# Performance work log

Hardware: AMD Instinct MI355X
Metric: run time of the kernel (lower is better)

## Reference

```python
import jax, jax.numpy as jnp
import numpy as np

DIM, HEADS, WS, SS = 256, 8, 4, 2
B, D, H, W = 2, 16, 56, 56


def _rel_pos_index(ws):
    coords = np.stack(np.meshgrid(np.arange(ws), np.arange(ws), np.arange(ws), indexing='ij'))
    flat = coords.reshape(3, -1)                      # [3, n]
    rel = (flat[:, :, None] - flat[:, None, :]).transpose(1, 2, 0).astype(np.int64)  # [n,n,3]
    rel[..., 0] += ws - 1; rel[..., 1] += ws - 1; rel[..., 2] += ws - 1
    rel[..., 0] *= (2 * ws - 1) ** 2
    rel[..., 1] *= (2 * ws - 1)
    return rel.sum(-1)                                # [n, n]


def _attn_mask(d, h, w, ws, ss):
    # dims are divisible by ws here, so padded dims == dims (matches torch ceil-pad)
    img = np.zeros((d, h, w))
    sl = (slice(0, -ws), slice(-ws, -ss), slice(-ss, None))
    cnt = 0
    for dsl in sl:
        for hsl in sl:
            for wsl in sl:
                img[dsl, hsl, wsl] = cnt
                cnt += 1
    mw = img.reshape(d // ws, ws, h // ws, ws, w // ws, ws)
    mw = mw.transpose(0, 2, 4, 1, 3, 5).reshape(-1, ws ** 3)   # [nW, n]
    diff = mw[:, None, :] - mw[:, :, None]
    return np.where(diff != 0, -100.0, 0.0).astype(np.float32)  # [nW, n, n]


def _window_partition(x, ws):
    b, d, h, w, c = x.shape
    x = x.reshape(b, d // ws, ws, h // ws, ws, w // ws, ws, c)
    return x.transpose(0, 1, 3, 5, 2, 4, 6, 7).reshape(-1, ws ** 3, c)


def _window_reverse(win, ws, b, d, h, w, c):
    x = win.reshape(b, d // ws, h // ws, w // ws, ws, ws, ws, c)
    return x.transpose(0, 1, 4, 2, 5, 3, 6, 7).reshape(b, d, h, w, c)


def _ln(x, g, b, eps=1e-5):
    mu = x.mean(-1, keepdims=True)
    var = ((x - mu) ** 2).mean(-1, keepdims=True)
    return (x - mu) * jax.lax.rsqrt(var + eps) * g + b


def setup_inputs() -> dict:
    key = jax.random.key(0)
    ks = jax.random.split(key, 8)
    s = 0.02
    return {
        'x': jax.random.normal(ks[0], (B, D, H, W, DIM), jnp.float32),
        'norm1_g': jnp.ones((DIM,), jnp.float32),
        'norm1_b': jnp.zeros((DIM,), jnp.float32),
        'qkv_w': jax.random.normal(ks[1], (DIM, 3 * DIM), jnp.float32) * s,
        'qkv_b': jnp.zeros((3 * DIM,), jnp.float32),
        'proj_w': jax.random.normal(ks[2], (DIM, DIM), jnp.float32) * s,
        'proj_b': jnp.zeros((DIM,), jnp.float32),
        'rpb_table': jax.random.normal(ks[3], ((2 * WS - 1) ** 3, HEADS), jnp.float32) * s,
        'norm2_g': jnp.ones((DIM,), jnp.float32),
        'norm2_b': jnp.zeros((DIM,), jnp.float32),
        'fc1_w': jax.random.normal(ks[4], (DIM, 4 * DIM), jnp.float32) * s,
        'fc1_b': jnp.zeros((4 * DIM,), jnp.float32),
        'fc2_w': jax.random.normal(ks[5], (4 * DIM, DIM), jnp.float32) * s,
        'fc2_b': jnp.zeros((DIM,), jnp.float32),
    }


def reference(x, norm1_g, norm1_b, qkv_w, qkv_b, proj_w, proj_b, rpb_table,
              norm2_g, norm2_b, fc1_w, fc1_b, fc2_w, fc2_b):
    b, d, h, w, c = x.shape
    nh, ws, ss = HEADS, WS, SS
    hd = c // nh
    shortcut = x

    xn = _ln(x, norm1_g, norm1_b)
    xs = jnp.roll(xn, shift=(-ss, -ss, -ss), axis=(1, 2, 3))
    xw = _window_partition(xs, ws)            # [B_, n, c]
    B_, n, _ = xw.shape

    qkv = (xw @ qkv_w + qkv_b).reshape(B_, n, 3, nh, hd).transpose(2, 0, 3, 1, 4)
    q, k, v = qkv[0], qkv[1], qkv[2]          # [B_, nh, n, hd]
    attn = jnp.einsum('bhqd,bhkd->bhqk', q * (hd ** -0.5), k)

    rpi = jnp.asarray(_rel_pos_index(ws).reshape(-1))
    bias = rpb_table[rpi].reshape(n, n, nh).transpose(2, 0, 1)  # [nh, n, n]
    attn = attn + bias[None]

    mask = jnp.asarray(_attn_mask(d, h, w, ws, ss))             # [nW, n, n]
    nW = mask.shape[0]
    attn = attn.reshape(B_ // nW, nW, nh, n, n) + mask[None, :, None]
    attn = jax.nn.softmax(attn.reshape(B_, nh, n, n), axis=-1)

    out = jnp.einsum('bhqk,bhkd->bhqd', attn, v).transpose(0, 2, 1, 3).reshape(B_, n, c)
    out = out @ proj_w + proj_b

    xr = _window_reverse(out, ws, b, d, h, w, c)
    xr = jnp.roll(xr, shift=(ss, ss, ss), axis=(1, 2, 3))
    x1 = shortcut + xr

    y = _ln(x1, norm2_g, norm2_b)
    y = jax.nn.gelu(y @ fc1_w + fc1_b, approximate=False) @ fc2_w + fc2_b
    return x1 + y
```

## Files before the change

### kernel.cpp

```cpp
#include <hip/hip_runtime.h>
#include <math.h>


using f32x4  = __attribute__((ext_vector_type(4))) float;
using bf16x8 = __attribute__((ext_vector_type(8))) short;

#define MFMA16 __builtin_amdgcn_mfma_f32_16x16x32_bf16

__device__ __forceinline__ short f2bf(float f) {
  unsigned u = __builtin_bit_cast(unsigned, f);
  u += 0x7fffu + ((u >> 16) & 1u);
  return (short)(u >> 16);
}

__device__ __forceinline__ float gelu_f(float v) {
  const float u = 1.5957691216057308f * v * (1.f + 0.044715f * v * v);
  const float e = __expf(u);
  return v - v * __builtin_amdgcn_rcpf(e + 1.f);
}

#define GLDS16(g, l) __builtin_amdgcn_global_load_lds(                        \
    (__attribute__((address_space(1))) void*)(g),                             \
    (__attribute__((address_space(3))) void*)(l), 16, 0, 0)

__global__ void transpose_all_k(const float* __restrict__ qkv_w,
                                const float* __restrict__ proj_w,
                                const float* __restrict__ fc1_w,
                                const float* __restrict__ fc2_w,
                                short* __restrict__ o_qkv,
                                short* __restrict__ o_proj,
                                short* __restrict__ o_fc1,
                                short* __restrict__ o_fc2) {
  int bid = blockIdx.x;
  const float* in; short* out; int K, N;
  if (bid < 768)       { in = qkv_w;  out = o_qkv;  K = 256;  N = 768; }
  else if (bid < 1024) { in = proj_w; out = o_proj; K = 256;  N = 256;  bid -= 768; }
  else if (bid < 2048) { in = fc1_w;  out = o_fc1;  K = 256;  N = 1024; bid -= 1024; }
  else                 { in = fc2_w;  out = o_fc2;  K = 1024; N = 256;  bid -= 2048; }
  const int idx = bid * 256 + threadIdx.x;
  const int k = idx / N, n = idx % N;
  out[(size_t)n * K + k] = f2bf(in[idx]);
}

__global__ __launch_bounds__(256) void ln1_part_k(
    const float* __restrict__ x, const float* __restrict__ g,
    const float* __restrict__ bta, short* __restrict__ xw) {
  const int wave = threadIdx.x >> 6, lane = threadIdx.x & 63;
  const int row = blockIdx.x * 4 + wave;
  const int win = row >> 6, tok = row & 63;
  const int b = win / 784, wi = win % 784;
  const int wd = wi / 196, wh = (wi / 14) % 14, ww = wi % 14;
  const int tz = tok >> 4, ty = (tok >> 2) & 3, tx = tok & 3;
  const int gd = (wd * 4 + tz + 2) & 15;
  int gh = wh * 4 + ty + 2; if (gh >= 56) gh -= 56;
  int gw = ww * 4 + tx + 2; if (gw >= 56) gw -= 56;
  const size_t src = ((((size_t)b * 16 + gd) * 56 + gh) * 56 + gw) * 256;
  const float4 v = ((const float4*)(x + src))[lane];
  float s = v.x + v.y + v.z + v.w;
#pragma unroll
  for (int m = 1; m < 64; m <<= 1) s += __shfl_xor(s, m);
  const float mean = s * (1.f / 256.f);
  const float dx = v.x - mean, dy = v.y - mean, dz = v.z - mean, dw = v.w - mean;
  float q = dx * dx + dy * dy + dz * dz + dw * dw;
#pragma unroll
  for (int m = 1; m < 64; m <<= 1) q += __shfl_xor(q, m);
  const float rstd = rsqrtf(q * (1.f / 256.f) + 1e-5f);
  const float4 gg = ((const float4*)g)[lane];
  const float4 bb = ((const float4*)bta)[lane];
  short4 o;
  o.x = f2bf(dx * rstd * gg.x + bb.x);
  o.y = f2bf(dy * rstd * gg.y + bb.y);
  o.z = f2bf(dz * rstd * gg.z + bb.z);
  o.w = f2bf(dw * rstd * gg.w + bb.w);
  *(short4*)(xw + (size_t)row * 256 + lane * 4) = o;
}

__global__ __launch_bounds__(256) void ln2_k(
    const float* __restrict__ x1, const float* __restrict__ g,
    const float* __restrict__ bta, short* __restrict__ yn) {
  const int wave = threadIdx.x >> 6, lane = threadIdx.x & 63;
  const int row = blockIdx.x * 4 + wave;
  const float4 v = ((const float4*)(x1 + (size_t)row * 256))[lane];
  float s = v.x + v.y + v.z + v.w;
#pragma unroll
  for (int m = 1; m < 64; m <<= 1) s += __shfl_xor(s, m);
  const float mean = s * (1.f / 256.f);
  const float dx = v.x - mean, dy = v.y - mean, dz = v.z - mean, dw = v.w - mean;
  float q = dx * dx + dy * dy + dz * dz + dw * dw;
#pragma unroll
  for (int m = 1; m < 64; m <<= 1) q += __shfl_xor(q, m);
  const float rstd = rsqrtf(q * (1.f / 256.f) + 1e-5f);
  const float4 gg = ((const float4*)g)[lane];
  const float4 bb = ((const float4*)bta)[lane];
  short4 o;
  o.x = f2bf(dx * rstd * gg.x + bb.x);
  o.y = f2bf(dy * rstd * gg.y + bb.y);
  o.z = f2bf(dz * rstd * gg.z + bb.z);
  o.w = f2bf(dw * rstd * gg.w + bb.w);
  *(short4*)(yn + (size_t)row * 256 + lane * 4) = o;
}

template <int EPI, int XSWZ>
__global__ __launch_bounds__(256) void gemm_k(
    const short* __restrict__ A, const short* __restrict__ Bt,
    const float* __restrict__ bias, const float* __restrict__ resid,
    void* __restrict__ OutP, int N, int K) {
  __shared__ short SMEM[32768];
  const int tid = threadIdx.x;
  const int wave = tid >> 6, lane = tid & 63;
  const int quad = lane >> 4, l15 = lane & 15;
  int m0, n0;
  if constexpr (XSWZ) {
    const int gx = gridDim.x;
    int lin = blockIdx.y * gx + blockIdx.x;
    const int q8 = (gx * gridDim.y) >> 3;
    lin = (lin & 7) * q8 + (lin >> 3);
    m0 = (lin / gx) * 128;
    n0 = (lin % gx) * 128;
  } else {
    m0 = blockIdx.y * 128;
    n0 = blockIdx.x * 128;
  }
  const int wm = (wave >> 1) * 64, wn = (wave & 1) * 64;

  f32x4 acc[4][4] = {};

  auto stage = [&](int b, int kk) {
    short* Asb = SMEM + b * 16384;
    short* Bsb = Asb + 8192;
#pragma unroll
    for (int i = 0; i < 4; ++i) {
      const int p = wave * 256 + i * 64 + lane;
      const int row = p >> 3;
      const int c = (p & 7) ^ (row & 7);
      GLDS16(A  + (size_t)(m0 + row) * K + (kk + c * 8),
             Asb + (size_t)(wave * 256 + i * 64) * 8);
      GLDS16(Bt + (size_t)(n0 + row) * K + (kk + c * 8),
             Bsb + (size_t)(wave * 256 + i * 64) * 8);
    }
  };
  auto compute = [&](int b) {
    const short* Asb = SMEM + b * 16384;
    const short* Bsb = Asb + 8192;
#pragma unroll
    for (int ks = 0; ks < 2; ++ks) {
      bf16x8 af[4], bfr[4];
#pragma unroll
      for (int t = 0; t < 4; ++t) {
        const int ra = wm + t * 16 + l15;
        const int ca = (ks * 4 + quad) ^ (ra & 7);
        af[t] = *(const bf16x8*)(Asb + ra * 64 + ca * 8);
        const int rb = wn + t * 16 + l15;
        const int cb = (ks * 4 + quad) ^ (rb & 7);
        bfr[t] = *(const bf16x8*)(Bsb + rb * 64 + cb * 8);
      }
#pragma unroll
      for (int mt = 0; mt < 4; ++mt)
#pragma unroll
        for (int nt = 0; nt < 4; ++nt)
          acc[mt][nt] = MFMA16(af[mt], bfr[nt], acc[mt][nt], 0, 0, 0);
    }
  };

  stage(0, 0);
  __syncthreads();
  int cur = 0;
  const int NT = K >> 6;
  for (int t = 0; t < NT - 1; ++t) {
    stage(cur ^ 1, (t + 1) * 64);
    compute(cur);
    __syncthreads();
    cur ^= 1;
  }
  compute(cur);

  __syncthreads();
  if constexpr (EPI == 0 || EPI == 1) {
#pragma unroll
    for (int nt = 0; nt < 4; ++nt) {
      const int col = wn + nt * 16 + l15;
      const float bv = bias[n0 + col];
#pragma unroll
      for (int mt = 0; mt < 4; ++mt)
#pragma unroll
        for (int reg = 0; reg < 4; ++reg) {
          const int row = wm + mt * 16 + quad * 4 + reg;
          float v = acc[mt][nt][reg] + bv;
          if constexpr (EPI == 1) v = gelu_f(v);
          const int byte = (row << 8) | ((col << 1) ^ ((row & 7) << 4));
          *(short*)((char*)SMEM + byte) = f2bf(v);
        }
    }
    __syncthreads();
    short* out = (short*)OutP;
#pragma unroll
    for (int i = 0; i < 8; ++i) {
      const int off = i * 4096 + tid * 16;
      const int row = off >> 8;
      const bf16x8 val =
          *(const bf16x8*)((char*)SMEM + (off ^ ((row & 7) << 4)));
      if constexpr (EPI == 0) {
        const int colg = n0 + ((off & 255) >> 1);
        const int gq = colg >> 8, rem = colg & 255;
        const int hh = rem >> 5, dd = rem & 31;
        const int grow = m0 + row;
        const int win = grow >> 6, tok = grow & 63;
        *(bf16x8*)(out + ((((size_t)win * 8 + hh) * 3 + gq) << 11)
                       + tok * 32 + dd) = val;
      } else {
        *(bf16x8*)(out + (size_t)(m0 + row) * N + n0 + ((off & 255) >> 1)) = val;
      }
    }
  } else {
    float* out = (float*)OutP;
#pragma unroll
    for (int hh = 0; hh < 2; ++hh) {
      if (hh) __syncthreads();
      if (wm == hh * 64) {
#pragma unroll
        for (int nt = 0; nt < 4; ++nt) {
          const int col = wn + nt * 16 + l15;
          const float bv = bias[n0 + col];
#pragma unroll
          for (int mt = 0; mt < 4; ++mt)
#pragma unroll
            for (int reg = 0; reg < 4; ++reg) {
              const int rloc = mt * 16 + quad * 4 + reg;
              const int byte = (rloc << 9) | ((col << 2) ^ ((rloc & 7) << 4));
              *(float*)((char*)SMEM + byte) = acc[mt][nt][reg] + bv;
            }
        }
      }
      __syncthreads();
#pragma unroll
      for (int i = 0; i < 8; ++i) {
        const int off = i * 4096 + tid * 16;
        const int rloc = off >> 9;
        f32x4 val = *(const f32x4*)((char*)SMEM + (off ^ ((rloc & 7) << 4)));
        const int colf = (off & 511) >> 2;
        const int grow = m0 + hh * 64 + rloc;
        size_t dst;
        if constexpr (EPI == 2) {
          const int win = grow >> 6, tok = grow & 63;
          const int b = win / 784, wi = win % 784;
          const int wd = wi / 196, wh = (wi / 14) % 14, ww = wi % 14;
          const int tz = tok >> 4, ty = (tok >> 2) & 3, tx = tok & 3;
          const int gd = (wd * 4 + tz + 2) & 15;
          int gh = wh * 4 + ty + 2; if (gh >= 56) gh -= 56;
          int gw = ww * 4 + tx + 2; if (gw >= 56) gw -= 56;
          dst = ((((size_t)b * 16 + gd) * 56 + gh) * 56 + gw) * 256
                + n0 + colf;
        } else {
          dst = (size_t)grow * 256 + n0 + colf;
        }
        const f32x4 r = *(const f32x4*)(resid + dst);
        val = val + r;
        *(f32x4*)(out + dst) = val;
      }
    }
  }
}

__global__ __launch_bounds__(256) void attn_k(
    const short* __restrict__ qkv, const float* __restrict__ rpb,
    short* __restrict__ aout) {
  __shared__ short Plds[4 * 64 * 80];
  const int tid = threadIdx.x;
  const int wave = tid >> 6, lane = tid & 63;
  const int quad = lane >> 4, l15 = lane & 15;
  const int win = blockIdx.x >> 1;
  const int h = ((blockIdx.x & 1) << 2) + wave;
  const int wi = win % 784;
  const int wd = wi / 196, wh = (wi / 14) % 14, ww = wi % 14;
  const short* base = qkv + ((((size_t)win * 8 + h) * 3) << 11);

  bf16x8 qf[4], kf[4];
#pragma unroll
  for (int t = 0; t < 4; ++t) {
    qf[t] = *(const bf16x8*)(base + (t * 16 + l15) * 32 + quad * 8);
    kf[t] = *(const bf16x8*)(base + 2048 + (t * 16 + l15) * 32 + quad * 8);
  }
  f32x4 S[4][4] = {};
#pragma unroll
  for (int mt = 0; mt < 4; ++mt)
#pragma unroll
    for (int nt = 0; nt < 4; ++nt)
      S[mt][nt] = MFMA16(qf[mt], kf[nt], S[mt][nt], 0, 0, 0);

  const bool bd = (wd == 3), bh = (wh == 13), bw = (ww == 13);
  const int yc = l15 >> 2, xc = l15 & 3;
  int labc[4];
#pragma unroll
  for (int nt = 0; nt < 4; ++nt) {
    const int rd = bd ? (nt < 2 ? 1 : 2) : 0;
    const int rh = bh ? (yc < 2 ? 1 : 2) : 0;
    const int rw = bw ? (xc < 2 ? 1 : 2) : 0;
    labc[nt] = rd * 9 + rh * 3 + rw;
  }
  const float scale = 0.17677669529663687f;
#pragma unroll
  for (int mt = 0; mt < 4; ++mt) {
    const int rdr = bd ? (mt < 2 ? 1 : 2) : 0;
    const int rhr = bh ? (quad < 2 ? 1 : 2) : 0;
#pragma unroll
    for (int reg = 0; reg < 4; ++reg) {
      const int rwr = bw ? (reg < 2 ? 1 : 2) : 0;
      const int labr = rdr * 9 + rhr * 3 + rwr;
      float sc[4];
#pragma unroll
      for (int nt = 0; nt < 4; ++nt) {
        const int rpi = (mt - nt + 3) * 49 + (quad - yc + 3) * 7 + (reg - xc + 3);
        const float bias = rpb[rpi * 8 + h];
        const float mv = (labr == labc[nt]) ? 0.f : -100.f;
        sc[nt] = S[mt][nt][reg] * scale + bias + mv;
      }
      float mx = fmaxf(fmaxf(sc[0], sc[1]), fmaxf(sc[2], sc[3]));
      mx = fmaxf(mx, __shfl_xor(mx, 1));
      mx = fmaxf(mx, __shfl_xor(mx, 2));
      mx = fmaxf(mx, __shfl_xor(mx, 4));
      mx = fmaxf(mx, __shfl_xor(mx, 8));
      float p[4], sum = 0.f;
#pragma unroll
      for (int nt = 0; nt < 4; ++nt) { p[nt] = __expf(sc[nt] - mx); sum += p[nt]; }
      sum += __shfl_xor(sum, 1);
      sum += __shfl_xor(sum, 2);
      sum += __shfl_xor(sum, 4);
      sum += __shfl_xor(sum, 8);
      const float inv = 1.f / sum;
      const int r = mt * 16 + quad * 4 + reg;
#pragma unroll
      for (int nt = 0; nt < 4; ++nt)
        Plds[(wave * 64 + r) * 80 + nt * 16 + l15] = f2bf(p[nt] * inv);
    }
  }

  bf16x8 vf[2][2];
#pragma unroll
  for (int kt = 0; kt < 2; ++kt)
#pragma unroll
    for (int n2 = 0; n2 < 2; ++n2)
#pragma unroll
      for (int j = 0; j < 8; ++j)
        vf[kt][n2][j] =
            base[4096 + (kt * 32 + quad * 8 + j) * 32 + n2 * 16 + l15];

  f32x4 O[4][2] = {};
#pragma unroll
  for (int mt = 0; mt < 4; ++mt) {
    const short* pr = &Plds[(wave * 64 + mt * 16 + l15) * 80 + quad * 8];
    const bf16x8 pa0 = *(const bf16x8*)pr;
    const bf16x8 pa1 = *(const bf16x8*)(pr + 32);
#pragma unroll
    for (int n2 = 0; n2 < 2; ++n2) {
      O[mt][n2] = MFMA16(pa0, vf[0][n2], O[mt][n2], 0, 0, 0);
      O[mt][n2] = MFMA16(pa1, vf[1][n2], O[mt][n2], 0, 0, 0);
    }
  }
#pragma unroll
  for (int mt = 0; mt < 4; ++mt)
#pragma unroll
    for (int n2 = 0; n2 < 2; ++n2)
#pragma unroll
      for (int reg = 0; reg < 4; ++reg) {
        const int tok = mt * 16 + quad * 4 + reg;
        aout[((size_t)win * 64 + tok) * 256 + h * 32 + n2 * 16 + l15] =
            f2bf(O[mt][n2][reg]);
      }
}

extern "C" void kernel_launch(void* const* d_in, const int* in_sizes, int n_in,
                              void* d_out, int out_size, void* d_ws,
                              size_t ws_size, hipStream_t stream) {
  const float* x      = (const float*)d_in[0];
  const float* n1g    = (const float*)d_in[1];
  const float* n1b    = (const float*)d_in[2];
  const float* qkv_w  = (const float*)d_in[3];
  const float* qkv_b  = (const float*)d_in[4];
  const float* proj_w = (const float*)d_in[5];
  const float* proj_b = (const float*)d_in[6];
  const float* rpb    = (const float*)d_in[7];
  const float* n2g    = (const float*)d_in[8];
  const float* n2b    = (const float*)d_in[9];
  const float* fc1_w  = (const float*)d_in[10];
  const float* fc1_b  = (const float*)d_in[11];
  const float* fc2_w  = (const float*)d_in[12];
  const float* fc2_b  = (const float*)d_in[13];

  char* ws = (char*)d_ws;
  short* wt_qkv  = (short*)(ws + 0);
  short* wt_proj = (short*)(ws + 393216);
  short* wt_fc1  = (short*)(ws + 524288);
  short* wt_fc2  = (short*)(ws + 1048576);
  short* bufS    = (short*)(ws + 1572864);
  short* bufL    = (short*)(ws + 52953088);
  float* x1      = (float*)d_out;

  transpose_all_k<<<3072, 256, 0, stream>>>(qkv_w, proj_w, fc1_w, fc2_w,
                                            wt_qkv, wt_proj, wt_fc1, wt_fc2);
  ln1_part_k<<<25088, 256, 0, stream>>>(x, n1g, n1b, bufS);
  gemm_k<0, 0><<<dim3(6, 784), 256, 0, stream>>>(bufS, wt_qkv, qkv_b, nullptr,
                                                 bufL, 768, 256);
  attn_k<<<3136, 256, 0, stream>>>(bufL, rpb, bufS);
  gemm_k<2, 0><<<dim3(2, 784), 256, 0, stream>>>(bufS, wt_proj, proj_b, x,
                                                 x1, 256, 256);
  ln2_k<<<25088, 256, 0, stream>>>(x1, n2g, n2b, bufS);
  gemm_k<1, 1><<<dim3(8, 784), 256, 0, stream>>>(bufS, wt_fc1, fc1_b, nullptr,
                                                 bufL, 1024, 256);
  gemm_k<3, 0><<<dim3(2, 784), 256, 0, stream>>>(bufL, wt_fc2, fc2_b, x1,
                                                 x1, 256, 1024);
}
```

Before: 659.7 us.

## Fuse fc1+GELU+fc2 MLP into one kernel keeping hidden activations in LDS

Replaces the separate fc1 (with GELU) and fc2 GEMM launches with a single fused MLP kernel. Each block handles 64 rows, computes 128-wide hidden chunks into LDS, applies GELU, and accumulates fc2 directly, so the large bf16 hidden tensor never round-trips through global memory. The fc1/fc2 weights are pre-packed into an MFMA fragment layout in the transpose kernel so they can be read straight from global/L2 without LDS staging. The cost is less weight reuse per block, since each 64-row block rereads the full weight set, plus extra syncs per hidden chunk.

```diff
diff --git a/kernel.cpp b/kernel.cpp
--- a/kernel.cpp
+++ b/kernel.cpp
@@ -31,15 +31,38 @@
                                 short* __restrict__ o_proj,
                                 short* __restrict__ o_fc1,
                                 short* __restrict__ o_fc2) {
-  int bid = blockIdx.x;
-  const float* in; short* out; int K, N;
-  if (bid < 768)       { in = qkv_w;  out = o_qkv;  K = 256;  N = 768; }
-  else if (bid < 1024) { in = proj_w; out = o_proj; K = 256;  N = 256;  bid -= 768; }
-  else if (bid < 2048) { in = fc1_w;  out = o_fc1;  K = 256;  N = 1024; bid -= 1024; }
-  else                 { in = fc2_w;  out = o_fc2;  K = 1024; N = 256;  bid -= 2048; }
-  const int idx = bid * 256 + threadIdx.x;
-  const int k = idx / N, n = idx % N;
-  out[(size_t)n * K + k] = f2bf(in[idx]);
+  const int bid = blockIdx.x;
+  if (bid < 768) {
+    const int idx = bid * 256 + threadIdx.x;
+    const int k = idx / 768, n = idx % 768;
+    o_qkv[(size_t)n * 256 + k] = f2bf(qkv_w[idx]);
+  } else if (bid < 1024) {
+    const int idx = (bid - 768) * 256 + threadIdx.x;
+    const int k = idx >> 8, n = idx & 255;
+    o_proj[(size_t)n * 256 + k] = f2bf(proj_w[idx]);
+  } else if (bid < 1152) {
+    const int idx = (bid - 1024) * 256 + threadIdx.x;
+    const int lane = idx & 63, rest = idx >> 6;
+    const int kt = rest & 7, ct = rest >> 3;
+    const int kb = kt * 32 + (lane >> 4) * 8;
+    const int n = ct * 16 + (lane & 15);
+    bf16x8 o;
+#pragma unroll
+    for (int j = 0; j < 8; ++j)
+      o[j] = f2bf(fc1_w[(size_t)(kb + j) * 1024 + n]);
+    *(bf16x8*)(o_fc1 + (size_t)idx * 8) = o;
+  } else {
+    const int idx = (bid - 1152) * 256 + threadIdx.x;
+    const int lane = idx & 63, rest = idx >> 6;
+    const int kt = rest & 31, ct = rest >> 5;
+    const int kb = kt * 32 + (lane >> 4) * 8;
+    const int n = ct * 16 + (lane & 15);
+    bf16x8 o;
+#pragma unroll
+    for (int j = 0; j < 8; ++j)
+      o[j] = f2bf(fc2_w[(size_t)(kb + j) * 256 + n]);
+    *(bf16x8*)(o_fc2 + (size_t)idx * 8) = o;
+  }
 }
 
 __global__ __launch_bounds__(256) void ln1_part_k(
@@ -175,7 +198,7 @@
   compute(cur);
 
   __syncthreads();
-  if constexpr (EPI == 0 || EPI == 1) {
+  if constexpr (EPI == 0) {
 #pragma unroll
     for (int nt = 0; nt < 4; ++nt) {
       const int col = wn + nt * 16 + l15;
@@ -185,10 +208,8 @@
 #pragma unroll
         for (int reg = 0; reg < 4; ++reg) {
           const int row = wm + mt * 16 + quad * 4 + reg;
-          float v = acc[mt][nt][reg] + bv;
-          if constexpr (EPI == 1) v = gelu_f(v);
           const int byte = (row << 8) | ((col << 1) ^ ((row & 7) << 4));
-          *(short*)((char*)SMEM + byte) = f2bf(v);
+          *(short*)((char*)SMEM + byte) = f2bf(acc[mt][nt][reg] + bv);
         }
     }
     __syncthreads();
@@ -199,17 +220,13 @@
       const int row = off >> 8;
       const bf16x8 val =
           *(const bf16x8*)((char*)SMEM + (off ^ ((row & 7) << 4)));
-      if constexpr (EPI == 0) {
-        const int colg = n0 + ((off & 255) >> 1);
-        const int gq = colg >> 8, rem = colg & 255;
-        const int hh = rem >> 5, dd = rem & 31;
-        const int grow = m0 + row;
-        const int win = grow >> 6, tok = grow & 63;
-        *(bf16x8*)(out + ((((size_t)win * 8 + hh) * 3 + gq) << 11)
-                       + tok * 32 + dd) = val;
-      } else {
-        *(bf16x8*)(out + (size_t)(m0 + row) * N + n0 + ((off & 255) >> 1)) = val;
-      }
+      const int colg = n0 + ((off & 255) >> 1);
+      const int gq = colg >> 8, rem = colg & 255;
+      const int hh = rem >> 5, dd = rem & 31;
+      const int grow = m0 + row;
+      const int win = grow >> 6, tok = grow & 63;
+      *(bf16x8*)(out + ((((size_t)win * 8 + hh) * 3 + gq) << 11)
+                     + tok * 32 + dd) = val;
     }
   } else {
     float* out = (float*)OutP;
@@ -239,24 +256,133 @@
         f32x4 val = *(const f32x4*)((char*)SMEM + (off ^ ((rloc & 7) << 4)));
         const int colf = (off & 511) >> 2;
         const int grow = m0 + hh * 64 + rloc;
-        size_t dst;
-        if constexpr (EPI == 2) {
-          const int win = grow >> 6, tok = grow & 63;
-          const int b = win / 784, wi = win % 784;
-          const int wd = wi / 196, wh = (wi / 14) % 14, ww = wi % 14;
-          const int tz = tok >> 4, ty = (tok >> 2) & 3, tx = tok & 3;
-          const int gd = (wd * 4 + tz + 2) & 15;
-          int gh = wh * 4 + ty + 2; if (gh >= 56) gh -= 56;
-          int gw = ww * 4 + tx + 2; if (gw >= 56) gw -= 56;
-          dst = ((((size_t)b * 16 + gd) * 56 + gh) * 56 + gw) * 256
-                + n0 + colf;
-        } else {
-          dst = (size_t)grow * 256 + n0 + colf;
-        }
+        const int win = grow >> 6, tok = grow & 63;
+        const int b = win / 784, wi = win % 784;
+        const int wd = wi / 196, wh = (wi / 14) % 14, ww = wi % 14;
+        const int tz = tok >> 4, ty = (tok >> 2) & 3, tx = tok & 3;
+        const int gd = (wd * 4 + tz + 2) & 15;
+        int gh = wh * 4 + ty + 2; if (gh >= 56) gh -= 56;
+        int gw = ww * 4 + tx + 2; if (gw >= 56) gw -= 56;
+        const size_t dst = ((((size_t)b * 16 + gd) * 56 + gh) * 56 + gw) * 256
+                           + n0 + colf;
         const f32x4 r = *(const f32x4*)(resid + dst);
         val = val + r;
         *(f32x4*)(out + dst) = val;
       }
+    }
+  }
+}
+
+__global__ __launch_bounds__(256, 3) void mlp2_k(
+    const short* __restrict__ yn, const short* __restrict__ W1f,
+    const short* __restrict__ W2f, const float* __restrict__ b1,
+    const float* __restrict__ b2, const float* __restrict__ resid,
+    float* __restrict__ out) {
+  __shared__ __align__(16) char SM[49152];
+  const int tid = threadIdx.x;
+  const int wave = tid >> 6, lane = tid & 63;
+  const int quad = lane >> 4, l15 = lane & 15;
+  const int m0 = blockIdx.x * 64;
+
+#pragma unroll
+  for (int i = 0; i < 8; ++i) {
+    const int p = i * 256 + tid;
+    const int row = p >> 5;
+    const int c = (p & 31) ^ (row & 7);
+    GLDS16(yn + (size_t)(m0 + row) * 256 + c * 8, SM + p * 16);
+  }
+  __syncthreads();
+
+  f32x4 oacc[4][4] = {};
+  for (int j = 0; j < 8; ++j) {
+    f32x4 hacc[4][2] = {};
+#pragma unroll
+    for (int kk = 0; kk < 8; ++kk) {
+      bf16x8 af[4];
+#pragma unroll
+      for (int mt = 0; mt < 4; ++mt) {
+        const int t = mt * 16 + l15;
+        af[mt] = *(const bf16x8*)(
+            SM + t * 512 + (((kk * 4 + quad) ^ (t & 7)) << 4));
+      }
+#pragma unroll
+      for (int ct = 0; ct < 2; ++ct) {
+        const int ctg = j * 8 + wave * 2 + ct;
+        const bf16x8 w1 = *(const bf16x8*)(
+            W1f + (size_t)((ctg * 8 + kk) * 64 + lane) * 8);
+#pragma unroll
+        for (int mt = 0; mt < 4; ++mt)
+          hacc[mt][ct] = MFMA16(af[mt], w1, hacc[mt][ct], 0, 0, 0);
+      }
+    }
+    if (j) __syncthreads();
+#pragma unroll
+    for (int ct = 0; ct < 2; ++ct) {
+      const int hc = wave * 32 + ct * 16 + l15;
+      const float bv = b1[j * 128 + hc];
+#pragma unroll
+      for (int mt = 0; mt < 4; ++mt)
+#pragma unroll
+        for (int reg = 0; reg < 4; ++reg) {
+          const int row = mt * 16 + quad * 4 + reg;
+          const float v = gelu_f(hacc[mt][ct][reg] + bv);
+          const int byte =
+              32768 + row * 256 + (((hc >> 3) ^ (row & 7)) << 4) + (hc & 7) * 2;
+          *(short*)(SM + byte) = f2bf(v);
+        }
+    }
+    __syncthreads();
+#pragma unroll
+    for (int kk2 = 0; kk2 < 4; ++kk2) {
+      bf16x8 ah[4];
+#pragma unroll
+      for (int mt = 0; mt < 4; ++mt) {
+        const int t = mt * 16 + l15;
+        ah[mt] = *(const bf16x8*)(
+            SM + 32768 + t * 256 + (((kk2 * 4 + quad) ^ (t & 7)) << 4));
+      }
+#pragma unroll
+      for (int nt = 0; nt < 4; ++nt) {
+        const int ct2 = wave * 4 + nt;
+        const bf16x8 w2 = *(const bf16x8*)(
+            W2f + (size_t)((ct2 * 32 + j * 4 + kk2) * 64 + lane) * 8);
+#pragma unroll
+        for (int mt = 0; mt < 4; ++mt)
+          oacc[mt][nt] = MFMA16(ah[mt], w2, oacc[mt][nt], 0, 0, 0);
+      }
+    }
+  }
+
+#pragma unroll
+  for (int hh = 0; hh < 2; ++hh) {
+    __syncthreads();
+#pragma unroll
+    for (int mi = 0; mi < 2; ++mi) {
+      const int mt = hh * 2 + mi;
+#pragma unroll
+      for (int nt = 0; nt < 4; ++nt) {
+        const int col = wave * 64 + nt * 16 + l15;
+        const float bv = b2[col];
+#pragma unroll
+        for (int reg = 0; reg < 4; ++reg) {
+          const int rl = mi * 16 + quad * 4 + reg;
+          const int byte =
+              rl * 1024 + (((col >> 2) ^ (rl & 7)) << 4) + (col & 3) * 4;
+          *(float*)(SM + byte) = oacc[mt][nt][reg] + bv;
+        }
+      }
+    }
+    __syncthreads();
+#pragma unroll
+    for (int i = 0; i < 8; ++i) {
+      const int off = i * 4096 + tid * 16;
+      const int rloc = off >> 10, w = off & 1023;
+      const int byte = rloc * 1024 + (((w >> 4) ^ (rloc & 7)) << 4);
+      f32x4 v = *(const f32x4*)(SM + byte);
+      const size_t dst = (size_t)(m0 + hh * 32 + rloc) * 256 + (w >> 2);
+      const f32x4 r = *(const f32x4*)(resid + dst);
+      v = v + r;
+      *(f32x4*)(out + dst) = v;
     }
   }
 }
@@ -395,7 +521,7 @@
   short* bufL    = (short*)(ws + 52953088);
   float* x1      = (float*)d_out;
 
-  transpose_all_k<<<3072, 256, 0, stream>>>(qkv_w, proj_w, fc1_w, fc2_w,
+  transpose_all_k<<<1280, 256, 0, stream>>>(qkv_w, proj_w, fc1_w, fc2_w,
                                             wt_qkv, wt_proj, wt_fc1, wt_fc2);
   ln1_part_k<<<25088, 256, 0, stream>>>(x, n1g, n1b, bufS);
   gemm_k<0, 0><<<dim3(6, 784), 256, 0, stream>>>(bufS, wt_qkv, qkv_b, nullptr,
@@ -404,8 +530,6 @@
   gemm_k<2, 0><<<dim3(2, 784), 256, 0, stream>>>(bufS, wt_proj, proj_b, x,
                                                  x1, 256, 256);
   ln2_k<<<25088, 256, 0, stream>>>(x1, n2g, n2b, bufS);
-  gemm_k<1, 1><<<dim3(8, 784), 256, 0, stream>>>(bufS, wt_fc1, fc1_b, nullptr,
-                                                 bufL, 1024, 256);
-  gemm_k<3, 0><<<dim3(2, 784), 256, 0, stream>>>(bufL, wt_fc2, fc2_b, x1,
-                                                 x1, 256, 1024);
-}
+  mlp2_k<<<1568, 256, 0, stream>>>(bufS, wt_fc1, wt_fc2, fc1_b, fc2_b,
+                                   x1, x1);
+}
```

New measurement: 951.2 us. 1.44x slower.
